# Optimization experiments

Measured on AMD Instinct MI355X. Metric: run time of the kernel, lower is better.

Reference implementation:

```python
import jax, jax.numpy as jnp
import numpy as np

EPS = 1e-5
B, T, D, V, NB, C, R, MT = 2, 256, 2048, 32000, 4, 512, 32, 3


def ste_sign_vec(w):
    alpha = jnp.mean(jnp.abs(w))
    hard = alpha * jnp.sign(w)
    hard = jnp.where(hard == 0, alpha, hard)
    return w + jax.lax.stop_gradient(hard - w)


def ste_sign(w):
    alpha = jnp.mean(jnp.abs(w), axis=-1, keepdims=True)
    hard = alpha * jnp.sign(w)
    hard = jnp.where(hard == 0, alpha, hard)
    return w + jax.lax.stop_gradient(hard - w)


def layernorm(x, g, b):
    m = jnp.mean(x, axis=-1, keepdims=True)
    v = jnp.var(x, axis=-1, keepdims=True)
    return (x - m) * jax.lax.rsqrt(v + EPS) * g + b


def hdc_block(x, i, decay_logit, bv_q, bv_k, bv_v, rules, query_bind, logic_gate,
              ln_mem_g, ln_mem_b, ln_attn_g, ln_attn_b, ln_logic_g, ln_logic_b,
              ctrl_ln_g, ctrl_ln_b, down_w, down_b, up_w, up_b):
    t = jnp.arange(T)
    # --- EMA memory (conv1d with decay^k kernel == lower-tri decay matmul) ---
    decay = jax.nn.sigmoid(decay_logit[i])
    expnt = t[:, None] - t[None, :]                     # (T,T)
    A = jnp.where(expnt >= 0, decay ** jnp.maximum(expnt, 0).astype(x.dtype), 0.0)
    mem = jnp.einsum('ts,bsd->btd', A, x)
    x = layernorm(x + mem, ln_mem_g[i], ln_mem_b[i])
    # --- sigmoid-gated boolean causal attention ---
    Q = x * ste_sign_vec(bv_q[i])
    K = x * ste_sign_vec(bv_k[i])
    Vv = x * ste_sign_vec(bv_v[i])
    scores = jnp.einsum('btd,bsd->bts', Q, K) * (D ** -0.5)
    causal = t[:, None] >= t[None, :]
    attn = jnp.where(causal[None], jax.nn.sigmoid(scores * 4.0), 0.0)
    att_out = jnp.einsum('bts,bsd->btd', attn, Vv)
    x = layernorm(x + att_out, ln_attn_g[i], ln_attn_b[i])
    # --- logic layer: sum_r w_r * (x*rule_r) == x * (w @ rules) ---
    rls = ste_sign(rules[i])                            # (R,D)
    query = x * ste_sign_vec(query_bind[i])
    sim = jnp.einsum('btd,rd->btr', query, rls) * (D ** -0.5)
    rw = jax.nn.sigmoid(sim * 4.0)
    logic_out = x * jnp.einsum('btr,rd->btd', rw, rls)
    gate = jax.nn.sigmoid(logic_gate[i])
    x = layernorm(x + gate * (logic_out - x), ln_logic_g[i], ln_logic_b[i])
    # --- controller MLP (dropout inactive in eval) ---
    h = layernorm(x, ctrl_ln_g[i], ctrl_ln_b[i])
    h = jax.nn.gelu(h @ down_w[i].T + down_b[i], approximate=False)
    h = h @ up_w[i].T + up_b[i]
    return x + h


def setup_inputs() -> dict:
    key = jax.random.key(0)
    ks = jax.random.split(key, 12)
    nrm = jax.random.normal
    return {
        'idx': jax.random.randint(ks[0], (B, T), 0, V),
        'codebook': 0.02 * nrm(ks[1], (V, D)),
        'decay_logit': jnp.full((NB,), 2.0),
        'bv_q': 0.5 * nrm(ks[2], (NB, D)),
        'bv_k': 0.5 * nrm(ks[3], (NB, D)),
        'bv_v': 0.5 * nrm(ks[4], (NB, D)),
        'rules': 0.5 * nrm(ks[5], (NB, R, D)),
        'query_bind': 0.5 * nrm(ks[6], (NB, D)),
        'logic_gate': jnp.full((NB,), -1.0),
        'ln_mem_g': jnp.ones((NB, D)), 'ln_mem_b': jnp.zeros((NB, D)),
        'ln_attn_g': jnp.ones((NB, D)), 'ln_attn_b': jnp.zeros((NB, D)),
        'ln_logic_g': jnp.ones((NB, D)), 'ln_logic_b': jnp.zeros((NB, D)),
        'ctrl_ln_g': jnp.ones((NB, D)), 'ctrl_ln_b': jnp.zeros((NB, D)),
        'down_w': nrm(ks[7], (NB, C, D)) / np.sqrt(D), 'down_b': jnp.zeros((NB, C)),
        'up_w': nrm(ks[8], (NB, D, C)) / np.sqrt(C), 'up_b': jnp.zeros((NB, D)),
        'tl_gates': jnp.zeros((MT,)),
        'tl_pos': 0.01 * nrm(ks[9], (MT, D)),
        'tl_ln_g': jnp.ones((D,)), 'tl_ln_b': jnp.zeros((D,)),
        'out_ln_g': jnp.ones((D,)), 'out_ln_b': jnp.zeros((D,)),
        'output_scale': jnp.array(1.0),
    }


def reference(idx, codebook, decay_logit, bv_q, bv_k, bv_v, rules, query_bind,
              logic_gate, ln_mem_g, ln_mem_b, ln_attn_g, ln_attn_b, ln_logic_g,
              ln_logic_b, ctrl_ln_g, ctrl_ln_b, down_w, down_b, up_w, up_b,
              tl_gates, tl_pos, tl_ln_g, tl_ln_b, out_ln_g, out_ln_b, output_scale):
    blk = (decay_logit, bv_q, bv_k, bv_v, rules, query_bind, logic_gate,
           ln_mem_g, ln_mem_b, ln_attn_g, ln_attn_b, ln_logic_g, ln_logic_b,
           ctrl_ln_g, ctrl_ln_b, down_w, down_b, up_w, up_b)

    def run_blocks(h):
        for i in range(NB):
            h = hdc_block(h, i, *blk)
        return h

    # encode: STE bipolar codebook + cyclic permutation positional binding
    tokens = ste_sign(jnp.take(codebook, idx, axis=0))  # (B,T,D)
    perm = (jnp.arange(D)[None, :] - jnp.arange(T)[:, None]) % D  # (T,D)
    tokens = jnp.take_along_axis(tokens, jnp.broadcast_to(perm[None], tokens.shape), axis=2)

    h = run_blocks(tokens)
    for ti in range(1, MT):  # thought loop (n_thoughts = max_thoughts)
        gate = jax.nn.sigmoid(tl_gates[ti])
        thought = run_blocks(layernorm(h, tl_ln_g, tl_ln_b) + tl_pos[ti])
        h = h + gate * (thought - h)

    h = layernorm(h, out_ln_g, out_ln_b)
    logits = (h @ codebook.T) * output_scale  # (B,T,V) weight-tied decoder
    return logits
```

## Files before the change

### kernel.cpp

```cpp
#include <hip/hip_runtime.h>
#include <math.h>

#define TT   256
#define DD   2048
#define VV   32000
#define NBLK 4
#define CC   512
#define RR   32
#define MTT  3
#define NBAT 2
#define NTOK 512

typedef unsigned int u32;
typedef unsigned short ushort_t;
typedef __attribute__((ext_vector_type(8))) short s16x8;
typedef __attribute__((ext_vector_type(4))) float f32x4;

__device__ __forceinline__ float sigm(float x){ return 1.0f/(1.0f+expf(-x)); }

__device__ __forceinline__ ushort_t f2bf(float f){
  u32 u = __float_as_uint(f);
  u32 r = (u + 0x7fffu + ((u >> 16) & 1u)) >> 16;
  return (ushort_t)r;
}
__device__ __forceinline__ float bf2f(ushort_t u){
  return __uint_as_float(((u32)u) << 16);
}

__device__ __forceinline__ void async_copy16(void* lds, const void* g){
  __builtin_amdgcn_global_load_lds((const __attribute__((address_space(1))) u32*)g,
                                   (__attribute__((address_space(3))) u32*)lds, 16, 0, 0);
}

__device__ __forceinline__ float block_sum256(float v){
  #pragma unroll
  for (int off = 32; off > 0; off >>= 1) v += __shfl_down(v, off);
  __shared__ float sh[4];
  __syncthreads();
  if ((threadIdx.x & 63) == 0) sh[threadIdx.x >> 6] = v;
  __syncthreads();
  return sh[0] + sh[1] + sh[2] + sh[3];
}

__global__ __launch_bounds__(256) void cvt2_kernel(const float* __restrict__ a,
    ushort_t* __restrict__ oa, long na4,
    const float* __restrict__ b, ushort_t* __restrict__ ob, long nb4){
  long i = (long)blockIdx.x * 256 + threadIdx.x;
  long stride = (long)gridDim.x * 256;
  long tot = na4 + nb4;
  for (; i < tot; i += stride){
    const float* src = (i < na4) ? a : b;
    ushort_t* dst = (i < na4) ? oa : ob;
    long k = (i < na4) ? i : i - na4;
    float4 v = ((const float4*)src)[k];
    ushort4 o;
    o.x = f2bf(v.x); o.y = f2bf(v.y); o.z = f2bf(v.z); o.w = f2bf(v.w);
    ((ushort4*)dst)[k] = o;
  }
}

__global__ __launch_bounds__(256) void sign_prep_kernel(
    const float* __restrict__ bv_q, const float* __restrict__ bv_k,
    const float* __restrict__ bv_v, const float* __restrict__ query_bind,
    const float* __restrict__ rules,
    float* __restrict__ SQK, float* __restrict__ SV, float* __restrict__ SQB,
    ushort_t* __restrict__ RLSb){
  int b = blockIdx.x;
  if (b < NBLK){
    const float* q = bv_q + (size_t)b * DD;
    const float* k = bv_k + (size_t)b * DD;
    float sq = 0.f, sk = 0.f;
    #pragma unroll
    for (int j = 0; j < 8; j++){
      int d = threadIdx.x + j*256;
      sq += fabsf(q[d]); sk += fabsf(k[d]);
    }
    float aq = block_sum256(sq) * (1.f/DD);
    float ak = block_sum256(sk) * (1.f/DD);
    float a2 = aq * ak;
    float* o = SQK + (size_t)b * DD;
    #pragma unroll
    for (int j = 0; j < 8; j++){
      int d = threadIdx.x + j*256;
      o[d] = ((q[d] < 0.f) != (k[d] < 0.f)) ? -a2 : a2;
    }
    return;
  }
  const float* w; float* of = nullptr; ushort_t* ob = nullptr;
  if (b < 2*NBLK){ w = bv_v + (size_t)(b - NBLK) * DD; of = SV + (size_t)(b - NBLK) * DD; }
  else if (b < 3*NBLK){ w = query_bind + (size_t)(b - 2*NBLK) * DD; of = SQB + (size_t)(b - 2*NBLK) * DD; }
  else { int r = b - 3*NBLK; w = rules + (size_t)r * DD; ob = RLSb + (size_t)r * DD; }
  float s = 0.f;
  #pragma unroll
  for (int j = 0; j < 8; j++) s += fabsf(w[threadIdx.x + j*256]);
  float a = block_sum256(s) * (1.f/DD);
  #pragma unroll
  for (int j = 0; j < 8; j++){
    int d = threadIdx.x + j*256;
    float v = (w[d] < 0.f) ? -a : a;
    if (of) of[d] = v;
    else    ob[d] = f2bf(v);
  }
}

__global__ __launch_bounds__(256) void encode_kernel(const int* __restrict__ idx,
    const float* __restrict__ cb, float* __restrict__ X, ushort_t* __restrict__ Xrb){
  int token = blockIdx.x;
  int t = token & (TT - 1);
  size_t row = (size_t)idx[token] * DD;
  float s = 0.f;
  #pragma unroll
  for (int j = 0; j < 8; j++) s += fabsf(cb[row + threadIdx.x + j*256]);
  float a = block_sum256(s) * (1.f/DD);
  #pragma unroll
  for (int j = 0; j < 8; j++){
    int d = threadIdx.x + j*256;
    float w = cb[row + ((d - t) & (DD - 1))];
    float v = (w < 0.f) ? -a : a;
    X[(size_t)token * DD + d] = v;
    Xrb[(size_t)token * DD + d] = f2bf(v);
  }
}

__global__ __launch_bounds__(256) void adec_kernel(const float* __restrict__ decay_logit,
    ushort_t* __restrict__ Adec){
  int i = blockIdx.y, t = blockIdx.x, s = threadIdx.x;
  float decay = sigm(decay_logit[i]);
  float l2 = log2f(decay);
  int e = t - s;
  float v = (e < 0) ? 0.f : exp2f((float)e * l2);
  Adec[((size_t)i*TT + t)*TT + s] = f2bf(v);
}

__global__ __launch_bounds__(256) void ln_kernel(const float* __restrict__ A,
    const float* __restrict__ g, const float* __restrict__ be,
    float* __restrict__ out, ushort_t* __restrict__ outb,
    const float* __restrict__ qscale, ushort_t* __restrict__ outq,
    const float* __restrict__ vscale, ushort_t* __restrict__ outv){
  size_t row = blockIdx.x;
  const float* a = A + row * DD;
  float vals[8]; float s = 0.f, ss = 0.f;
  #pragma unroll
  for (int j = 0; j < 8; j++){
    int d = threadIdx.x + j*256;
    float v = a[d];
    vals[j] = v; s += v; ss += v*v;
  }
  float mean = block_sum256(s) * (1.f/DD);
  float var  = block_sum256(ss) * (1.f/DD) - mean*mean;
  float inv  = rsqrtf(var + 1e-5f);
  #pragma unroll
  for (int j = 0; j < 8; j++){
    int d = threadIdx.x + j*256;
    float y = (vals[j] - mean) * inv * g[d] + be[d];
    if (out)  out[row*DD + d] = y;
    if (outb) outb[row*DD + d] = f2bf(y);
    if (outq) outq[row*DD + d] = f2bf(y * qscale[d]);
    if (outv) outv[row*DD + d] = f2bf(y * vscale[d]);
  }
}

__global__ __launch_bounds__(256) void fuse_logic_kernel(const float* __restrict__ T0,
    const ushort_t* __restrict__ RLSi, const float* __restrict__ SQBi,
    const float* __restrict__ g2, const float* __restrict__ b2,
    const float* __restrict__ gate_ptr,
    const float* __restrict__ g3, const float* __restrict__ b3,
    const float* __restrict__ g4, const float* __restrict__ b4,
    float* __restrict__ X, ushort_t* __restrict__ T1b){
  __shared__ float sh[256*33];
  __shared__ float red[8*32];
  __shared__ float rwsh[32];
  const float RSD = 0.022097086912079608f;
  int tid = threadIdx.x;
  size_t tok = blockIdx.x;
  const float* a = T0 + tok * DD;
  float v[8]; float s = 0.f, ss = 0.f;
  #pragma unroll
  for (int j = 0; j < 8; j++){
    int d = tid + 256*j;
    v[j] = a[d]; s += v[j]; ss += v[j]*v[j];
  }
  float mean = block_sum256(s) * (1.f/DD);
  float var  = block_sum256(ss) * (1.f/DD) - mean*mean;
  float inv  = rsqrtf(var + 1e-5f);
  float y2[8], xq[8];
  #pragma unroll
  for (int j = 0; j < 8; j++){
    int d = tid + 256*j;
    y2[j] = (v[j] - mean) * inv * g2[d] + b2[d];
    xq[j] = y2[j] * SQBi[d];
  }
  float aa[32];
  #pragma unroll 4
  for (int r = 0; r < 32; r++){
    float t = 0.f;
    #pragma unroll
    for (int j = 0; j < 8; j++)
      t = fmaf(xq[j], bf2f(RLSi[(size_t)r*DD + tid + 256*j]), t);
    aa[r] = t;
  }
  #pragma unroll
  for (int r = 0; r < 32; r++) sh[tid*33 + r] = aa[r];
  __syncthreads();
  {
    int r = tid & 31, gg = tid >> 5;
    float t = 0.f;
    #pragma unroll 8
    for (int i = 0; i < 32; i++) t += sh[(gg*32 + i)*33 + r];
    red[gg*32 + r] = t;
  }
  __syncthreads();
  if (tid < 32){
    float t = 0.f;
    #pragma unroll
    for (int gg = 0; gg < 8; gg++) t += red[gg*32 + tid];
    rwsh[tid] = sigm(4.f * RSD * t);
  }
  __syncthreads();
  float gate = sigm(*gate_ptr);
  float p3[8]; s = 0.f; ss = 0.f;
  #pragma unroll
  for (int j = 0; j < 8; j++){
    int d = tid + 256*j;
    float t = 0.f;
    #pragma unroll 8
    for (int r = 0; r < 32; r++)
      t = fmaf(rwsh[r], bf2f(RLSi[(size_t)r*DD + d]), t);
    float lo = y2[j] * t;
    p3[j] = y2[j] + gate * (lo - y2[j]);
    s += p3[j]; ss += p3[j]*p3[j];
  }
  mean = block_sum256(s) * (1.f/DD);
  var  = block_sum256(ss) * (1.f/DD) - mean*mean;
  inv  = rsqrtf(var + 1e-5f);
  float y3[8]; s = 0.f; ss = 0.f;
  #pragma unroll
  for (int j = 0; j < 8; j++){
    int d = tid + 256*j;
    y3[j] = (p3[j] - mean) * inv * g3[d] + b3[d];
    X[tok*DD + d] = y3[j];
    s += y3[j]; ss += y3[j]*y3[j];
  }
  mean = block_sum256(s) * (1.f/DD);
  var  = block_sum256(ss) * (1.f/DD) - mean*mean;
  inv  = rsqrtf(var + 1e-5f);
  #pragma unroll
  for (int j = 0; j < 8; j++){
    int d = tid + 256*j;
    T1b[tok*DD + d] = f2bf((y3[j] - mean) * inv * g4[d] + b4[d]);
  }
}

__global__ __launch_bounds__(256) void tl_kernel(const float* __restrict__ Xr,
    float* __restrict__ H, const float* __restrict__ gate_ptr,
    const float* __restrict__ g, const float* __restrict__ be,
    const float* __restrict__ pos,
    float* __restrict__ outX, ushort_t* __restrict__ outXb){
  size_t row = blockIdx.x;
  float gate = gate_ptr ? sigm(*gate_ptr) : 1.f;
  float v[8]; float s = 0.f, ss = 0.f;
  #pragma unroll
  for (int j = 0; j < 8; j++){
    int d = threadIdx.x + j*256;
    float xr = Xr[row*DD + d];
    float hv = gate_ptr ? H[row*DD + d] : 0.f;
    float hn = gate_ptr ? (hv + gate * (xr - hv)) : xr;
    H[row*DD + d] = hn;
    v[j] = hn; s += hn; ss += hn*hn;
  }
  float mean = block_sum256(s) * (1.f/DD);
  float var  = block_sum256(ss) * (1.f/DD) - mean*mean;
  float inv  = rsqrtf(var + 1e-5f);
  #pragma unroll
  for (int j = 0; j < 8; j++){
    int d = threadIdx.x + j*256;
    float y = (v[j] - mean) * inv * g[d] + be[d];
    if (pos) y += pos[d];
    if (outX)  outX[row*DD + d] = y;
    if (outXb) outXb[row*DD + d] = f2bf(y);
  }
}

template<int BM, int BN, int SPLITK, int ACT, bool CAUSAL, bool OUTBF>
__global__ __launch_bounds__(256) void gemm_nt(const ushort_t* __restrict__ A,
    const ushort_t* __restrict__ B, void* __restrict__ Cv,
    int K, int lda, int ldb, int ldc,
    long sA, long sB, long sC,
    const float* __restrict__ colscale, const float* __restrict__ bias,
    const float* __restrict__ res, ushort_t* __restrict__ mirror,
    const float* __restrict__ alpha_ptr, float alpha_c)
{
  constexpr int FM = BM / 32;
  constexpr int FN = BN / 32;
  __shared__ __align__(16) ushort_t shA[BM * 64];
  __shared__ __align__(16) ushort_t shB[BN * 64];
  const int tid = threadIdx.x;
  const int l = tid & 63, w = tid >> 6;
  const int wr = w >> 1, wc = w & 1;
  const int row0 = blockIdx.y * BM, col0 = blockIdx.x * BN;
  const int zb = blockIdx.z / SPLITK, zk = blockIdx.z % SPLITK;

  if (CAUSAL && col0 > row0 + BM - 1) return;

  A += (size_t)zb * sA;
  B += (size_t)zb * sB;
  const int kbeg = zk * (K / SPLITK), kend = kbeg + K / SPLITK;

  f32x4 acc[FM][FN] = {};

  for (int kt = kbeg; kt < kend; kt += 64){
    #pragma unroll
    for (int i = 0; i < BM/32; i++){
      int o = i*4096 + tid*16;
      int r = o >> 7, c = (o >> 4) & 7;
      int lc = c ^ (r & 7);
      async_copy16((char*)shA + o, A + (size_t)(row0 + r) * lda + kt + lc*8);
    }
    #pragma unroll
    for (int i = 0; i < BN/32; i++){
      int o = i*4096 + tid*16;
      int r = o >> 7, c = (o >> 4) & 7;
      int lc = c ^ (r & 7);
      async_copy16((char*)shB + o, B + (size_t)(col0 + r) * ldb + kt + lc*8);
    }
    __syncthreads();
    #pragma unroll
    for (int kk = 0; kk < 2; kk++){
      s16x8 af[FM], bfr[FN];
      #pragma unroll
      for (int mi = 0; mi < FM; mi++){
        int r = wr*(BM/2) + mi*16 + (l & 15);
        int c = kk*4 + (l >> 4);
        af[mi] = *(const s16x8*)((const char*)shA + r*128 + (c ^ (r & 7))*16);
      }
      #pragma unroll
      for (int ni = 0; ni < FN; ni++){
        int r = wc*(BN/2) + ni*16 + (l & 15);
        int c = kk*4 + (l >> 4);
        bfr[ni] = *(const s16x8*)((const char*)shB + r*128 + (c ^ (r & 7))*16);
      }
      #pragma unroll
      for (int mi = 0; mi < FM; mi++)
        #pragma unroll
        for (int ni = 0; ni < FN; ni++)
          acc[mi][ni] = __builtin_amdgcn_mfma_f32_16x16x32_bf16(af[mi], bfr[ni], acc[mi][ni], 0, 0, 0);
    }
    __syncthreads();
  }

  if (SPLITK > 1){
    float* P = (float*)Cv + (size_t)blockIdx.z * sC;
    #pragma unroll
    for (int mi = 0; mi < FM; mi++)
      #pragma unroll
      for (int ni = 0; ni < FN; ni++)
        #pragma unroll
        for (int j = 0; j < 4; j++){
          int m = row0 + wr*(BM/2) + mi*16 + (l >> 4)*4 + j;
          int n = col0 + wc*(BN/2) + ni*16 + (l & 15);
          P[(size_t)m * ldc + n] = acc[mi][ni][j];
        }
    return;
  }

  float alpha = alpha_c * (alpha_ptr ? *alpha_ptr : 1.f);
  float* Cf = (float*)Cv + (size_t)zb * sC;
  ushort_t* Cb = (ushort_t*)Cv + (size_t)zb * sC;
  const float* resz = res ? res + (size_t)zb * sC : nullptr;
  #pragma unroll
  for (int mi = 0; mi < FM; mi++){
    #pragma unroll
    for (int ni = 0; ni < FN; ni++){
      #pragma unroll
      for (int j = 0; j < 4; j++){
        int m = row0 + wr*(BM/2) + mi*16 + (l >> 4)*4 + j;
        int n = col0 + wc*(BN/2) + ni*16 + (l & 15);
        float v = acc[mi][ni][j] * alpha;
        if (colscale) v *= colscale[n];
        if (bias) v += bias[n];
        if (ACT == 1) v = sigm(4.f * v);
        else if (ACT == 2) v = 0.5f * v * (1.f + erff(v * 0.70710678118654752f));
        if (CAUSAL && n > m) v = 0.f;
        if (resz) v += resz[(size_t)m * ldc + n];
        if (OUTBF) Cb[(size_t)m * ldc + n] = f2bf(v);
        else       Cf[(size_t)m * ldc + n] = v;
        if (mirror) mirror[(size_t)m * ldc + n] = f2bf(v);
      }
    }
  }
}

__global__ __launch_bounds__(256) void gemm_nn(const ushort_t* __restrict__ A,
    const ushort_t* __restrict__ B, float* __restrict__ C,
    int K, int lda, int ldb, int ldc,
    long sA, long sB, long sC,
    const float* __restrict__ res)
{
  __shared__ __align__(16) ushort_t shA[64 * 64];
  __shared__ __align__(16) ushort_t shB[64 * 64];
  const int tid = threadIdx.x;
  const int l = tid & 63, w = tid >> 6;
  const int wr = w >> 1, wc = w & 1;
  const int row0 = blockIdx.y * 64, col0 = blockIdx.x * 64;
  A += (size_t)blockIdx.z * sA;
  B += (size_t)blockIdx.z * sB;

  const int kb = tid & 63;
  const int nb0 = (tid >> 6) * 8;

  f32x4 acc[2][2] = {};

  for (int kt = 0; kt < K; kt += 64){
    #pragma unroll
    for (int i = 0; i < 2; i++){
      int o = i*4096 + tid*16;
      int r = o >> 7, c = (o >> 4) & 7;
      int lc = c ^ (r & 7);
      async_copy16((char*)shA + o, A + (size_t)(row0 + r) * lda + kt + lc*8);
    }
    #pragma unroll
    for (int i = 0; i < 2; i++){
      int n0 = nb0 + i*32;
      s16x8 v = *(const s16x8*)(B + (size_t)(kt + kb) * ldb + col0 + n0);
      #pragma unroll
      for (int j = 0; j < 8; j++){
        int n = n0 + j;
        int off = n*128 + (((kb >> 3) ^ (n & 7)) << 4) + ((kb & 7) << 1);
        *(ushort_t*)((char*)shB + off) = (ushort_t)v[j];
      }
    }
    __syncthreads();
    #pragma unroll
    for (int kk = 0; kk < 2; kk++){
      s16x8 af[2], bfr[2];
      #pragma unroll
      for (int mi = 0; mi < 2; mi++){
        int r = wr*32 + mi*16 + (l & 15);
        int c = kk*4 + (l >> 4);
        af[mi] = *(const s16x8*)((const char*)shA + r*128 + ((c ^ (r & 7)) << 4));
      }
      #pragma unroll
      for (int ni = 0; ni < 2; ni++){
        int r = wc*32 + ni*16 + (l & 15);
        int c = kk*4 + (l >> 4);
        bfr[ni] = *(const s16x8*)((const char*)shB + r*128 + ((c ^ (r & 7)) << 4));
      }
      #pragma unroll
      for (int mi = 0; mi < 2; mi++)
        #pragma unroll
        for (int ni = 0; ni < 2; ni++)
          acc[mi][ni] = __builtin_amdgcn_mfma_f32_16x16x32_bf16(af[mi], bfr[ni], acc[mi][ni], 0, 0, 0);
    }
    __syncthreads();
  }

  float* Cf = C + (size_t)blockIdx.z * sC;
  const float* resz = res ? res + (size_t)blockIdx.z * sC : nullptr;
  #pragma unroll
  for (int mi = 0; mi < 2; mi++)
    #pragma unroll
    for (int ni = 0; ni < 2; ni++)
      #pragma unroll
      for (int j = 0; j < 4; j++){
        int m = row0 + wr*32 + mi*16 + (l >> 4)*4 + j;
        int n = col0 + wc*32 + ni*16 + (l & 15);
        float v = acc[mi][ni][j];
        if (resz) v += resz[(size_t)m * ldc + n];
        Cf[(size_t)m * ldc + n] = v;
      }
}

__global__ __launch_bounds__(256) void gemm_ntf(const ushort_t* __restrict__ A,
    const float* __restrict__ B, float* __restrict__ C,
    int K, int lda, int ldb, int ldc,
    const float* __restrict__ alpha_ptr)
{
  constexpr int BM = 256, BN = 64, FM = 8, FN = 2;
  __shared__ __align__(16) ushort_t shA[BM * 64];
  __shared__ __align__(16) ushort_t shB[BN * 64];
  const int tid = threadIdx.x;
  const int l = tid & 63, w = tid >> 6;
  const int wr = w >> 1, wc = w & 1;
  const int row0 = blockIdx.y * BM, col0 = blockIdx.x * BN;

  f32x4 acc[FM][FN] = {};

  for (int kt = 0; kt < K; kt += 64){
    #pragma unroll
    for (int i = 0; i < BM/32; i++){
      int o = i*4096 + tid*16;
      int r = o >> 7, c = (o >> 4) & 7;
      int lc = c ^ (r & 7);
      async_copy16((char*)shA + o, A + (size_t)(row0 + r) * lda + kt + lc*8);
    }
    #pragma unroll
    for (int i = 0; i < 4; i++){
      int c2 = tid + i*256;
      int r = c2 & 63, kq = c2 >> 6;
      float4 v = *(const float4*)(B + (size_t)(col0 + r) * ldb + kt + kq*4);
      u32 p0 = ((u32)f2bf(v.y) << 16) | (u32)f2bf(v.x);
      u32 p1 = ((u32)f2bf(v.w) << 16) | (u32)f2bf(v.z);
      int off = r*128 + (((kq >> 1) ^ (r & 7)) << 4) + ((kq & 1) << 3);
      uint2 pp; pp.x = p0; pp.y = p1;
      *(uint2*)((char*)shB + off) = pp;
    }
    __syncthreads();
    #pragma unroll
    for (int kk = 0; kk < 2; kk++){
      s16x8 af[FM], bfr[FN];
      #pragma unroll
      for (int mi = 0; mi < FM; mi++){
        int r = wr*(BM/2) + mi*16 + (l & 15);
        int c = kk*4 + (l >> 4);
        af[mi] = *(const s16x8*)((const char*)shA + r*128 + ((c ^ (r & 7)) << 4));
      }
      #pragma unroll
      for (int ni = 0; ni < FN; ni++){
        int r = wc*(BN/2) + ni*16 + (l & 15);
        int c = kk*4 + (l >> 4);
        bfr[ni] = *(const s16x8*)((const char*)shB + r*128 + ((c ^ (r & 7)) << 4));
      }
      #pragma unroll
      for (int mi = 0; mi < FM; mi++)
        #pragma unroll
        for (int ni = 0; ni < FN; ni++)
          acc[mi][ni] = __builtin_amdgcn_mfma_f32_16x16x32_bf16(af[mi], bfr[ni], acc[mi][ni], 0, 0, 0);
    }
    __syncthreads();
  }

  float alpha = *alpha_ptr;
  #pragma unroll
  for (int mi = 0; mi < FM; mi++)
    #pragma unroll
    for (int ni = 0; ni < FN; ni++)
      #pragma unroll
      for (int j = 0; j < 4; j++){
        int m = row0 + wr*(BM/2) + mi*16 + (l >> 4)*4 + j;
        int n = col0 + wc*(BN/2) + ni*16 + (l & 15);
        C[(size_t)m * ldc + n] = acc[mi][ni][j] * alpha;
      }
}

template<int S, int ACT, bool CAUSAL, bool OUTBF>
__global__ __launch_bounds__(256) void reduce_epi(const float* __restrict__ P,
    void* __restrict__ outv, int M, int N, const float* __restrict__ bias, float alpha){
  long MN = (long)M * N;
  long idx = ((long)blockIdx.x * 256 + threadIdx.x) * 4;
  int b = (int)(idx / MN);
  long r = idx - (long)b * MN;
  int m = (int)(r / N), n = (int)(r % N);
  float vv[4] = {0.f, 0.f, 0.f, 0.f};
  #pragma unroll
  for (int s = 0; s < S; s++){
    float4 p = *(const float4*)&P[((long)(b*S + s)) * MN + r];
    vv[0] += p.x; vv[1] += p.y; vv[2] += p.z; vv[3] += p.w;
  }
  ushort4 ob; float4 of;
  float* po = (float*)&of;
  ushort_t* pb = (ushort_t*)&ob;
  #pragma unroll
  for (int j = 0; j < 4; j++){
    float v = vv[j] * alpha;
    if (bias) v += bias[n + j];
    if (ACT == 1) v = sigm(4.f * v);
    else if (ACT == 2) v = 0.5f * v * (1.f + erff(v * 0.70710678118654752f));
    if (CAUSAL && n + j > m) v = 0.f;
    po[j] = v; pb[j] = f2bf(v);
  }
  if (OUTBF) *(ushort4*)&((ushort_t*)outv)[(long)b*MN + r] = ob;
  else       *(float4*)&((float*)outv)[(long)b*MN + r] = of;
}

extern "C" void kernel_launch(void* const* d_in, const int* in_sizes, int n_in,
                              void* d_out, int out_size, void* d_ws, size_t ws_size,
                              hipStream_t stream){
  const int*   idx        = (const int*)  d_in[0];
  const float* cb         = (const float*)d_in[1];
  const float* decay_lg   = (const float*)d_in[2];
  const float* bv_q       = (const float*)d_in[3];
  const float* bv_k       = (const float*)d_in[4];
  const float* bv_v       = (const float*)d_in[5];
  const float* rules      = (const float*)d_in[6];
  const float* query_bind = (const float*)d_in[7];
  const float* logic_gate = (const float*)d_in[8];
  const float* ln_mem_g   = (const float*)d_in[9];
  const float* ln_mem_b   = (const float*)d_in[10];
  const float* ln_attn_g  = (const float*)d_in[11];
  const float* ln_attn_b  = (const float*)d_in[12];
  const float* ln_logic_g = (const float*)d_in[13];
  const float* ln_logic_b = (const float*)d_in[14];
  const float* ctrl_g     = (const float*)d_in[15];
  const float* ctrl_b     = (const float*)d_in[16];
  const float* down_w     = (const float*)d_in[17];
  const float* down_b     = (const float*)d_in[18];
  const float* up_w       = (const float*)d_in[19];
  const float* up_b       = (const float*)d_in[20];
  const float* tl_gates   = (const float*)d_in[21];
  const float* tl_pos     = (const float*)d_in[22];
  const float* tl_g       = (const float*)d_in[23];
  const float* tl_b       = (const float*)d_in[24];
  const float* out_g      = (const float*)d_in[25];
  const float* out_b      = (const float*)d_in[26];
  const float* oscale     = (const float*)d_in[27];
  float* out = (float*)d_out;

  const size_t ND = (size_t)NTOK * DD;
  char* p = (char*)d_ws;
  auto alloc = [&](size_t bytes){ void* r = p; p += (bytes + 255) & ~(size_t)255; return r; };
  float*    X       = (float*)   alloc(ND * 4);
  float*    H       = (float*)   alloc(ND * 4);
  float*    T0      = (float*)   alloc(ND * 4);
  ushort_t* Xrb     = (ushort_t*)alloc(ND * 2);
  ushort_t* Xb      = (ushort_t*)alloc(ND * 2);
  ushort_t* Xqb     = (ushort_t*)alloc(ND * 2);
  ushort_t* Xvb     = (ushort_t*)alloc(ND * 2);
  ushort_t* T1b     = (ushort_t*)alloc(ND * 2);
  ushort_t* ATTNb   = (ushort_t*)alloc((size_t)NBAT * TT * TT * 2);
  ushort_t* CBb     = (ushort_t*)alloc((size_t)NTOK * CC * 2);
  float*    PP      = (float*)   alloc((size_t)8 * NTOK * CC * 4);
  float*    SQK     = (float*)   alloc((size_t)NBLK * DD * 4);
  float*    SV      = (float*)   alloc((size_t)NBLK * DD * 4);
  float*    SQB     = (float*)   alloc((size_t)NBLK * DD * 4);
  ushort_t* RLSb    = (ushort_t*)alloc((size_t)NBLK * RR * DD * 2);
  ushort_t* Adec    = (ushort_t*)alloc((size_t)NBLK * TT * TT * 2);
  ushort_t* down_wb = (ushort_t*)alloc((size_t)NBLK * CC * DD * 2);
  ushort_t* up_wb   = (ushort_t*)alloc((size_t)NBLK * DD * CC * 2);

  const float RSD = 0.022097086912079608f;

  sign_prep_kernel<<<3*NBLK + NBLK*RR, 256, 0, stream>>>(
      bv_q, bv_k, bv_v, query_bind, rules, SQK, SV, SQB, RLSb);
  adec_kernel<<<dim3(TT, NBLK), 256, 0, stream>>>(decay_lg, Adec);
  cvt2_kernel<<<2048, 256, 0, stream>>>(down_w, down_wb, (long)NBLK*CC*DD/4,
                                        up_w, up_wb, (long)NBLK*DD*CC/4);
  encode_kernel<<<NTOK, 256, 0, stream>>>(idx, cb, X, Xrb);

  auto run_blocks = [&](){
    for (int i = 0; i < NBLK; i++){
      const size_t iD = (size_t)i * DD;
      gemm_nn<<<dim3(DD/64, TT/64, NBAT), 256, 0, stream>>>(
          Adec + (size_t)i*TT*TT, Xrb, T0, TT, TT, DD, DD,
          0, (long)TT*DD, (long)TT*DD, X);
      ln_kernel<<<NTOK, 256, 0, stream>>>(T0, ln_mem_g + iD, ln_mem_b + iD,
          X, Xb, SQK + iD, Xqb, SV + iD, Xvb);
      gemm_nt<64,64,8,0,true,false><<<dim3(TT/64, TT/64, NBAT*8), 256, 0, stream>>>(
          Xqb, Xb, PP, DD, DD, DD, TT,
          (long)TT*DD, (long)TT*DD, (long)TT*TT,
          nullptr, nullptr, nullptr, nullptr, nullptr, 1.f);
      reduce_epi<8,1,true,true><<<(NBAT*TT*TT)/1024, 256, 0, stream>>>(
          PP, ATTNb, TT, TT, nullptr, RSD);
      gemm_nn<<<dim3(DD/64, TT/64, NBAT), 256, 0, stream>>>(
          ATTNb, Xvb, T0, TT, TT, DD, DD,
          (long)TT*TT, (long)TT*DD, (long)TT*DD, X);
      fuse_logic_kernel<<<NTOK, 256, 0, stream>>>(T0,
          RLSb + (size_t)i*RR*DD, SQB + iD,
          ln_attn_g + iD, ln_attn_b + iD, logic_gate + i,
          ln_logic_g + iD, ln_logic_b + iD, ctrl_g + iD, ctrl_b + iD,
          X, T1b);
      gemm_nt<64,64,8,0,false,false><<<dim3(CC/64, NTOK/64, 8), 256, 0, stream>>>(
          T1b, down_wb + (size_t)i*CC*DD, PP, DD, DD, DD, CC,
          0, 0, (long)NTOK*CC,
          nullptr, nullptr, nullptr, nullptr, nullptr, 1.f);
      reduce_epi<8,2,false,true><<<(NTOK*CC)/1024, 256, 0, stream>>>(
          PP, CBb, NTOK, CC, down_b + (size_t)i*CC, 1.f);
      gemm_nt<64,64,1,0,false,false><<<dim3(DD/64, NTOK/64, 1), 256, 0, stream>>>(
          CBb, up_wb + (size_t)i*DD*CC, X, CC, CC, CC, DD,
          0, 0, 0, nullptr, up_b + iD, X, Xrb, nullptr, 1.f);
    }
  };

  run_blocks();
  tl_kernel<<<NTOK, 256, 0, stream>>>(X, H, nullptr, tl_g, tl_b,
      tl_pos + (size_t)1*DD, X, Xrb);
  run_blocks();
  tl_kernel<<<NTOK, 256, 0, stream>>>(X, H, tl_gates + 1, tl_g, tl_b,
      tl_pos + (size_t)2*DD, X, Xrb);
  run_blocks();
  tl_kernel<<<NTOK, 256, 0, stream>>>(X, H, tl_gates + 2, out_g, out_b,
      nullptr, nullptr, T1b);
  gemm_ntf<<<dim3(VV/64, NTOK/256, 1), 256, 0, stream>>>(
      T1b, cb, out, DD, DD, DD, VV, oscale);
}
```

Measured before the change: 1.248 ms.

## Fuse split-K reductions into consumer GEMMs and pre-convert codebook for decoder GEMM

The split-K partial sums for attention scores and the MLP down projection are now reduced, activated and converted to bf16 inside the A-tile load of the following GEMMs (attn·V and up projection). This removes two reduce kernels and their intermediate buffers. The decay-matrix kernel is merged into the sign prep launch. The final vocab projection now converts the codebook to bf16 once in a separate pass, then runs the generic 128x128 bf16 NT GEMM instead of converting fp32 inside the tile loads. The cost is rereading the 8 partials once per column tile and a large extra conversion pass.

```diff
diff --git a/kernel.cpp b/kernel.cpp
--- a/kernel.cpp
+++ b/kernel.cpp
@@ -25,6 +25,9 @@
 }
 __device__ __forceinline__ float bf2f(ushort_t u){
   return __uint_as_float(((u32)u) << 16);
+}
+__device__ __forceinline__ float gelu(float v){
+  return 0.5f * v * (1.f + erff(v * 0.70710678118654752f));
 }
 
 __device__ __forceinline__ void async_copy16(void* lds, const void* g){
@@ -59,13 +62,35 @@
   }
 }
 
+__global__ __launch_bounds__(256) void cvt_bf16_kernel(const float* __restrict__ in,
+    ushort_t* __restrict__ out, long n4){
+  long i = (long)blockIdx.x * 256 + threadIdx.x;
+  long stride = (long)gridDim.x * 256;
+  for (; i < n4; i += stride){
+    float4 v = ((const float4*)in)[i];
+    ushort4 o;
+    o.x = f2bf(v.x); o.y = f2bf(v.y); o.z = f2bf(v.z); o.w = f2bf(v.w);
+    ((ushort4*)out)[i] = o;
+  }
+}
+
 __global__ __launch_bounds__(256) void sign_prep_kernel(
     const float* __restrict__ bv_q, const float* __restrict__ bv_k,
     const float* __restrict__ bv_v, const float* __restrict__ query_bind,
-    const float* __restrict__ rules,
+    const float* __restrict__ rules, const float* __restrict__ decay_logit,
     float* __restrict__ SQK, float* __restrict__ SV, float* __restrict__ SQB,
-    ushort_t* __restrict__ RLSb){
+    ushort_t* __restrict__ RLSb, ushort_t* __restrict__ Adec){
   int b = blockIdx.x;
+  if (b >= 3*NBLK + NBLK*RR){
+    int e = b - (3*NBLK + NBLK*RR);
+    int i = e >> 8, t = e & (TT - 1), s = threadIdx.x;
+    float decay = sigm(decay_logit[i]);
+    float l2 = log2f(decay);
+    int ex = t - s;
+    float v = (ex < 0) ? 0.f : exp2f((float)ex * l2);
+    Adec[((size_t)i*TT + t)*TT + s] = f2bf(v);
+    return;
+  }
   if (b < NBLK){
     const float* q = bv_q + (size_t)b * DD;
     const float* k = bv_k + (size_t)b * DD;
@@ -120,16 +145,6 @@
     X[(size_t)token * DD + d] = v;
     Xrb[(size_t)token * DD + d] = f2bf(v);
   }
-}
-
-__global__ __launch_bounds__(256) void adec_kernel(const float* __restrict__ decay_logit,
-    ushort_t* __restrict__ Adec){
-  int i = blockIdx.y, t = blockIdx.x, s = threadIdx.x;
-  float decay = sigm(decay_logit[i]);
-  float l2 = log2f(decay);
-  int e = t - s;
-  float v = (e < 0) ? 0.f : exp2f((float)e * l2);
-  Adec[((size_t)i*TT + t)*TT + s] = f2bf(v);
 }
 
 __global__ __launch_bounds__(256) void ln_kernel(const float* __restrict__ A,
@@ -331,13 +346,13 @@
       for (int mi = 0; mi < FM; mi++){
         int r = wr*(BM/2) + mi*16 + (l & 15);
         int c = kk*4 + (l >> 4);
-        af[mi] = *(const s16x8*)((const char*)shA + r*128 + (c ^ (r & 7))*16);
+        af[mi] = *(const s16x8*)((const char*)shA + r*128 + ((c ^ (r & 7)) << 4));
       }
       #pragma unroll
       for (int ni = 0; ni < FN; ni++){
         int r = wc*(BN/2) + ni*16 + (l & 15);
         int c = kk*4 + (l >> 4);
-        bfr[ni] = *(const s16x8*)((const char*)shB + r*128 + (c ^ (r & 7))*16);
+        bfr[ni] = *(const s16x8*)((const char*)shB + r*128 + ((c ^ (r & 7)) << 4));
       }
       #pragma unroll
       for (int mi = 0; mi < FM; mi++)
@@ -379,7 +394,7 @@
         if (colscale) v *= colscale[n];
         if (bias) v += bias[n];
         if (ACT == 1) v = sigm(4.f * v);
-        else if (ACT == 2) v = 0.5f * v * (1.f + erff(v * 0.70710678118654752f));
+        else if (ACT == 2) v = gelu(v);
         if (CAUSAL && n > m) v = 0.f;
         if (resz) v += resz[(size_t)m * ldc + n];
         if (OUTBF) Cb[(size_t)m * ldc + n] = f2bf(v);
@@ -470,106 +485,180 @@
       }
 }
 
-__global__ __launch_bounds__(256) void gemm_ntf(const ushort_t* __restrict__ A,
-    const float* __restrict__ B, float* __restrict__ C,
-    int K, int lda, int ldb, int ldc,
-    const float* __restrict__ alpha_ptr)
+__global__ __launch_bounds__(256) void gemm_attnv(const float* __restrict__ P,
+    const ushort_t* __restrict__ Bv, float* __restrict__ C,
+    const float* __restrict__ res)
 {
-  constexpr int BM = 256, BN = 64, FM = 8, FN = 2;
-  __shared__ __align__(16) ushort_t shA[BM * 64];
-  __shared__ __align__(16) ushort_t shB[BN * 64];
+  __shared__ __align__(16) ushort_t shA[64 * 64];
+  __shared__ __align__(16) ushort_t shB[64 * 64];
+  const float RSD = 0.022097086912079608f;
   const int tid = threadIdx.x;
   const int l = tid & 63, w = tid >> 6;
   const int wr = w >> 1, wc = w & 1;
-  const int row0 = blockIdx.y * BM, col0 = blockIdx.x * BN;
-
-  f32x4 acc[FM][FN] = {};
-
-  for (int kt = 0; kt < K; kt += 64){
-    #pragma unroll
-    for (int i = 0; i < BM/32; i++){
+  const int row0 = blockIdx.y * 64, col0 = blockIdx.x * 64;
+  const int zb = blockIdx.z;
+  const ushort_t* B = Bv + (size_t)zb * TT * DD;
+  const float* Pz = P + (size_t)zb * 8 * TT * TT;
+  const int ar = tid & 63, acq = tid >> 6;
+  const int kb = tid & 63, nb0 = (tid >> 6) * 8;
+
+  f32x4 acc[2][2] = {};
+
+  for (int kt = 0; kt < TT; kt += 64){
+    #pragma unroll
+    for (int q = 0; q < 4; q++){
+      int c = acq*16 + q*4;
+      const float* pp = Pz + (size_t)(row0 + ar) * TT + kt + c;
+      float4 s4 = *(const float4*)pp;
+      #pragma unroll
+      for (int s = 1; s < 8; s++){
+        float4 t4 = *(const float4*)(pp + (size_t)s * TT * TT);
+        s4.x += t4.x; s4.y += t4.y; s4.z += t4.z; s4.w += t4.w;
+      }
+      float vj[4] = {s4.x, s4.y, s4.z, s4.w};
+      u32 lo = 0, hi = 0;
+      #pragma unroll
+      for (int j = 0; j < 4; j++){
+        float v = (kt + c + j > row0 + ar) ? 0.f : sigm(4.f * RSD * vj[j]);
+        u32 bb = f2bf(v);
+        if (j < 2) lo |= bb << (16*j); else hi |= bb << (16*(j-2));
+      }
+      int off = ar*128 + ((((c >> 3)) ^ (ar & 7)) << 4) + ((c & 7) << 1);
+      uint2 pk; pk.x = lo; pk.y = hi;
+      *(uint2*)((char*)shA + off) = pk;
+    }
+    #pragma unroll
+    for (int i = 0; i < 2; i++){
+      int n0 = nb0 + i*32;
+      s16x8 v = *(const s16x8*)(B + (size_t)(kt + kb) * DD + col0 + n0);
+      #pragma unroll
+      for (int j = 0; j < 8; j++){
+        int n = n0 + j;
+        int off = n*128 + (((kb >> 3) ^ (n & 7)) << 4) + ((kb & 7) << 1);
+        *(ushort_t*)((char*)shB + off) = (ushort_t)v[j];
+      }
+    }
+    __syncthreads();
+    #pragma unroll
+    for (int kk = 0; kk < 2; kk++){
+      s16x8 af[2], bfr[2];
+      #pragma unroll
+      for (int mi = 0; mi < 2; mi++){
+        int r = wr*32 + mi*16 + (l & 15);
+        int c = kk*4 + (l >> 4);
+        af[mi] = *(const s16x8*)((const char*)shA + r*128 + ((c ^ (r & 7)) << 4));
+      }
+      #pragma unroll
+      for (int ni = 0; ni < 2; ni++){
+        int r = wc*32 + ni*16 + (l & 15);
+        int c = kk*4 + (l >> 4);
+        bfr[ni] = *(const s16x8*)((const char*)shB + r*128 + ((c ^ (r & 7)) << 4));
+      }
+      #pragma unroll
+      for (int mi = 0; mi < 2; mi++)
+        #pragma unroll
+        for (int ni = 0; ni < 2; ni++)
+          acc[mi][ni] = __builtin_amdgcn_mfma_f32_16x16x32_bf16(af[mi], bfr[ni], acc[mi][ni], 0, 0, 0);
+    }
+    __syncthreads();
+  }
+
+  float* Cf = C + (size_t)zb * TT * DD;
+  const float* rz = res + (size_t)zb * TT * DD;
+  #pragma unroll
+  for (int mi = 0; mi < 2; mi++)
+    #pragma unroll
+    for (int ni = 0; ni < 2; ni++)
+      #pragma unroll
+      for (int j = 0; j < 4; j++){
+        int m = row0 + wr*32 + mi*16 + (l >> 4)*4 + j;
+        int n = col0 + wc*32 + ni*16 + (l & 15);
+        Cf[(size_t)m * DD + n] = acc[mi][ni][j] + rz[(size_t)m * DD + n];
+      }
+}
+
+__global__ __launch_bounds__(256) void gemm_upf(const float* __restrict__ P,
+    const ushort_t* __restrict__ Bw, float* __restrict__ X,
+    const float* __restrict__ dnb, const float* __restrict__ upb,
+    ushort_t* __restrict__ mirror)
+{
+  __shared__ __align__(16) ushort_t shA[64 * 64];
+  __shared__ __align__(16) ushort_t shB[64 * 64];
+  const int tid = threadIdx.x;
+  const int l = tid & 63, w = tid >> 6;
+  const int wr = w >> 1, wc = w & 1;
+  const int row0 = blockIdx.y * 64, col0 = blockIdx.x * 64;
+  const int ar = tid & 63, acq = tid >> 6;
+
+  f32x4 acc[2][2] = {};
+
+  for (int kt = 0; kt < CC; kt += 64){
+    #pragma unroll
+    for (int q = 0; q < 4; q++){
+      int c = acq*16 + q*4;
+      const float* pp = P + (size_t)(row0 + ar) * CC + kt + c;
+      float4 s4 = *(const float4*)pp;
+      #pragma unroll
+      for (int s = 1; s < 8; s++){
+        float4 t4 = *(const float4*)(pp + (size_t)s * NTOK * CC);
+        s4.x += t4.x; s4.y += t4.y; s4.z += t4.z; s4.w += t4.w;
+      }
+      float vj[4] = {s4.x, s4.y, s4.z, s4.w};
+      u32 lo = 0, hi = 0;
+      #pragma unroll
+      for (int j = 0; j < 4; j++){
+        float v = gelu(vj[j] + dnb[kt + c + j]);
+        u32 bb = f2bf(v);
+        if (j < 2) lo |= bb << (16*j); else hi |= bb << (16*(j-2));
+      }
+      int off = ar*128 + ((((c >> 3)) ^ (ar & 7)) << 4) + ((c & 7) << 1);
+      uint2 pk; pk.x = lo; pk.y = hi;
+      *(uint2*)((char*)shA + off) = pk;
+    }
+    #pragma unroll
+    for (int i = 0; i < 2; i++){
       int o = i*4096 + tid*16;
       int r = o >> 7, c = (o >> 4) & 7;
       int lc = c ^ (r & 7);
-      async_copy16((char*)shA + o, A + (size_t)(row0 + r) * lda + kt + lc*8);
-    }
-    #pragma unroll
-    for (int i = 0; i < 4; i++){
-      int c2 = tid + i*256;
-      int r = c2 & 63, kq = c2 >> 6;
-      float4 v = *(const float4*)(B + (size_t)(col0 + r) * ldb + kt + kq*4);
-      u32 p0 = ((u32)f2bf(v.y) << 16) | (u32)f2bf(v.x);
-      u32 p1 = ((u32)f2bf(v.w) << 16) | (u32)f2bf(v.z);
-      int off = r*128 + (((kq >> 1) ^ (r & 7)) << 4) + ((kq & 1) << 3);
-      uint2 pp; pp.x = p0; pp.y = p1;
-      *(uint2*)((char*)shB + off) = pp;
+      async_copy16((char*)shB + o, Bw + (size_t)(col0 + r) * CC + kt + lc*8);
     }
     __syncthreads();
     #pragma unroll
     for (int kk = 0; kk < 2; kk++){
-      s16x8 af[FM], bfr[FN];
-      #pragma unroll
-      for (int mi = 0; mi < FM; mi++){
-        int r = wr*(BM/2) + mi*16 + (l & 15);
+      s16x8 af[2], bfr[2];
+      #pragma unroll
+      for (int mi = 0; mi < 2; mi++){
+        int r = wr*32 + mi*16 + (l & 15);
         int c = kk*4 + (l >> 4);
         af[mi] = *(const s16x8*)((const char*)shA + r*128 + ((c ^ (r & 7)) << 4));
       }
       #pragma unroll
-      for (int ni = 0; ni < FN; ni++){
-        int r = wc*(BN/2) + ni*16 + (l & 15);
+      for (int ni = 0; ni < 2; ni++){
+        int r = wc*32 + ni*16 + (l & 15);
         int c = kk*4 + (l >> 4);
         bfr[ni] = *(const s16x8*)((const char*)shB + r*128 + ((c ^ (r & 7)) << 4));
       }
       #pragma unroll
-      for (int mi = 0; mi < FM; mi++)
+      for (int mi = 0; mi < 2; mi++)
         #pragma unroll
-        for (int ni = 0; ni < FN; ni++)
+        for (int ni = 0; ni < 2; ni++)
           acc[mi][ni] = __builtin_amdgcn_mfma_f32_16x16x32_bf16(af[mi], bfr[ni], acc[mi][ni], 0, 0, 0);
     }
     __syncthreads();
   }
 
-  float alpha = *alpha_ptr;
-  #pragma unroll
-  for (int mi = 0; mi < FM; mi++)
-    #pragma unroll
-    for (int ni = 0; ni < FN; ni++)
+  #pragma unroll
+  for (int mi = 0; mi < 2; mi++)
+    #pragma unroll
+    for (int ni = 0; ni < 2; ni++)
       #pragma unroll
       for (int j = 0; j < 4; j++){
-        int m = row0 + wr*(BM/2) + mi*16 + (l >> 4)*4 + j;
-        int n = col0 + wc*(BN/2) + ni*16 + (l & 15);
-        C[(size_t)m * ldc + n] = acc[mi][ni][j] * alpha;
-      }
-}
-
-template<int S, int ACT, bool CAUSAL, bool OUTBF>
-__global__ __launch_bounds__(256) void reduce_epi(const float* __restrict__ P,
-    void* __restrict__ outv, int M, int N, const float* __restrict__ bias, float alpha){
-  long MN = (long)M * N;
-  long idx = ((long)blockIdx.x * 256 + threadIdx.x) * 4;
-  int b = (int)(idx / MN);
-  long r = idx - (long)b * MN;
-  int m = (int)(r / N), n = (int)(r % N);
-  float vv[4] = {0.f, 0.f, 0.f, 0.f};
-  #pragma unroll
-  for (int s = 0; s < S; s++){
-    float4 p = *(const float4*)&P[((long)(b*S + s)) * MN + r];
-    vv[0] += p.x; vv[1] += p.y; vv[2] += p.z; vv[3] += p.w;
-  }
-  ushort4 ob; float4 of;
-  float* po = (float*)&of;
-  ushort_t* pb = (ushort_t*)&ob;
-  #pragma unroll
-  for (int j = 0; j < 4; j++){
-    float v = vv[j] * alpha;
-    if (bias) v += bias[n + j];
-    if (ACT == 1) v = sigm(4.f * v);
-    else if (ACT == 2) v = 0.5f * v * (1.f + erff(v * 0.70710678118654752f));
-    if (CAUSAL && n + j > m) v = 0.f;
-    po[j] = v; pb[j] = f2bf(v);
-  }
-  if (OUTBF) *(ushort4*)&((ushort_t*)outv)[(long)b*MN + r] = ob;
-  else       *(float4*)&((float*)outv)[(long)b*MN + r] = of;
+        int m = row0 + wr*32 + mi*16 + (l >> 4)*4 + j;
+        int n = col0 + wc*32 + ni*16 + (l & 15);
+        float v = acc[mi][ni][j] + upb[n] + X[(size_t)m * DD + n];
+        X[(size_t)m * DD + n] = v;
+        mirror[(size_t)m * DD + n] = f2bf(v);
+      }
 }
 
 extern "C" void kernel_launch(void* const* d_in, const int* in_sizes, int n_in,
@@ -606,7 +695,10 @@
   float* out = (float*)d_out;
 
   const size_t ND = (size_t)NTOK * DD;
-  char* p = (char*)d_ws;
+  const size_t CBB = (size_t)VV * DD * 2;
+  char* base = (char*)d_ws;
+  ushort_t* cb_b = (ushort_t*)base;
+  char* p = base;
   auto alloc = [&](size_t bytes){ void* r = p; p += (bytes + 255) & ~(size_t)255; return r; };
   float*    X       = (float*)   alloc(ND * 4);
   float*    H       = (float*)   alloc(ND * 4);
@@ -615,9 +707,6 @@
   ushort_t* Xb      = (ushort_t*)alloc(ND * 2);
   ushort_t* Xqb     = (ushort_t*)alloc(ND * 2);
   ushort_t* Xvb     = (ushort_t*)alloc(ND * 2);
-  ushort_t* T1b     = (ushort_t*)alloc(ND * 2);
-  ushort_t* ATTNb   = (ushort_t*)alloc((size_t)NBAT * TT * TT * 2);
-  ushort_t* CBb     = (ushort_t*)alloc((size_t)NTOK * CC * 2);
   float*    PP      = (float*)   alloc((size_t)8 * NTOK * CC * 4);
   float*    SQK     = (float*)   alloc((size_t)NBLK * DD * 4);
   float*    SV      = (float*)   alloc((size_t)NBLK * DD * 4);
@@ -626,12 +715,10 @@
   ushort_t* Adec    = (ushort_t*)alloc((size_t)NBLK * TT * TT * 2);
   ushort_t* down_wb = (ushort_t*)alloc((size_t)NBLK * CC * DD * 2);
   ushort_t* up_wb   = (ushort_t*)alloc((size_t)NBLK * DD * CC * 2);
-
-  const float RSD = 0.022097086912079608f;
-
-  sign_prep_kernel<<<3*NBLK + NBLK*RR, 256, 0, stream>>>(
-      bv_q, bv_k, bv_v, query_bind, rules, SQK, SV, SQB, RLSb);
-  adec_kernel<<<dim3(TT, NBLK), 256, 0, stream>>>(decay_lg, Adec);
+  ushort_t* T1b = (ushort_t*)(base + CBB);
+
+  sign_prep_kernel<<<3*NBLK + NBLK*RR + NBLK*TT, 256, 0, stream>>>(
+      bv_q, bv_k, bv_v, query_bind, rules, decay_lg, SQK, SV, SQB, RLSb, Adec);
   cvt2_kernel<<<2048, 256, 0, stream>>>(down_w, down_wb, (long)NBLK*CC*DD/4,
                                         up_w, up_wb, (long)NBLK*DD*CC/4);
   encode_kernel<<<NTOK, 256, 0, stream>>>(idx, cb, X, Xrb);
@@ -648,11 +735,7 @@
           Xqb, Xb, PP, DD, DD, DD, TT,
           (long)TT*DD, (long)TT*DD, (long)TT*TT,
           nullptr, nullptr, nullptr, nullptr, nullptr, 1.f);
-      reduce_epi<8,1,true,true><<<(NBAT*TT*TT)/1024, 256, 0, stream>>>(
-          PP, ATTNb, TT, TT, nullptr, RSD);
-      gemm_nn<<<dim3(DD/64, TT/64, NBAT), 256, 0, stream>>>(
-          ATTNb, Xvb, T0, TT, TT, DD, DD,
-          (long)TT*TT, (long)TT*DD, (long)TT*DD, X);
+      gemm_attnv<<<dim3(DD/64, TT/64, NBAT), 256, 0, stream>>>(PP, Xvb, T0, X);
       fuse_logic_kernel<<<NTOK, 256, 0, stream>>>(T0,
           RLSb + (size_t)i*RR*DD, SQB + iD,
           ln_attn_g + iD, ln_attn_b + iD, logic_gate + i,
@@ -662,11 +745,9 @@
           T1b, down_wb + (size_t)i*CC*DD, PP, DD, DD, DD, CC,
           0, 0, (long)NTOK*CC,
           nullptr, nullptr, nullptr, nullptr, nullptr, 1.f);
-      reduce_epi<8,2,false,true><<<(NTOK*CC)/1024, 256, 0, stream>>>(
-          PP, CBb, NTOK, CC, down_b + (size_t)i*CC, 1.f);
-      gemm_nt<64,64,1,0,false,false><<<dim3(DD/64, NTOK/64, 1), 256, 0, stream>>>(
-          CBb, up_wb + (size_t)i*DD*CC, X, CC, CC, CC, DD,
-          0, 0, 0, nullptr, up_b + iD, X, Xrb, nullptr, 1.f);
+      gemm_upf<<<dim3(DD/64, NTOK/64, 1), 256, 0, stream>>>(
+          PP, up_wb + (size_t)i*DD*CC, X,
+          down_b + (size_t)i*CC, up_b + iD, Xrb);
     }
   };
 
@@ -679,6 +760,8 @@
   run_blocks();
   tl_kernel<<<NTOK, 256, 0, stream>>>(X, H, tl_gates + 2, out_g, out_b,
       nullptr, nullptr, T1b);
-  gemm_ntf<<<dim3(VV/64, NTOK/256, 1), 256, 0, stream>>>(
-      T1b, cb, out, DD, DD, DD, VV, oscale);
-}
+  cvt_bf16_kernel<<<4096, 256, 0, stream>>>(cb, cb_b, (long)VV*DD/4);
+  gemm_nt<128,128,1,0,false,false><<<dim3(VV/128, NTOK/128, 1), 256, 0, stream>>>(
+      T1b, cb_b, out, DD, DD, DD, VV,
+      0, 0, 0, nullptr, nullptr, nullptr, nullptr, oscale, 1.f);
+}
```

Measured after the change: 2.453 ms. +96.6%, slower.
